# Kernel tuning notes

Measured on AMD Instinct MI355X. Metric: run time of the kernel, lower is better.

## Reference

```python
import jax, jax.numpy as jnp
import numpy as np

B, S, D = 4, 2048, 1024
H, HD = 16, 64
F = 4096
EPS = 1e-5


def layer_norm(x, gamma, beta):
    mu = jnp.mean(x, axis=-1, keepdims=True)
    var = jnp.var(x, axis=-1, keepdims=True)
    return (x - mu) * jax.lax.rsqrt(var + EPS) * gamma + beta


def setup_inputs() -> dict:
    key = jax.random.key(0)
    ks = jax.random.split(key, 16)
    s_d = 1.0 / np.sqrt(D)
    s_hd = 1.0 / np.sqrt(H * HD)
    s_f = 1.0 / np.sqrt(F)
    return {
        "x": jax.random.normal(ks[0], (B, S, D), jnp.float32),
        # per-head Q/K/V linears stacked over heads: [H, D, HD]
        "Wq": jax.random.uniform(ks[1], (H, D, HD), jnp.float32, -s_d, s_d),
        "bq": jax.random.uniform(ks[2], (H, HD), jnp.float32, -s_d, s_d),
        "Wk": jax.random.uniform(ks[3], (H, D, HD), jnp.float32, -s_d, s_d),
        "bk": jax.random.uniform(ks[4], (H, HD), jnp.float32, -s_d, s_d),
        "Wv": jax.random.uniform(ks[5], (H, D, HD), jnp.float32, -s_d, s_d),
        "bv": jax.random.uniform(ks[6], (H, HD), jnp.float32, -s_d, s_d),
        "Wo": jax.random.uniform(ks[7], (H * HD, D), jnp.float32, -s_hd, s_hd),
        "bo": jax.random.uniform(ks[8], (D,), jnp.float32, -s_hd, s_hd),
        "W1": jax.random.uniform(ks[9], (D, F), jnp.float32, -s_d, s_d),
        "b1": jax.random.uniform(ks[10], (F,), jnp.float32, -s_d, s_d),
        "W2": jax.random.uniform(ks[11], (F, D), jnp.float32, -s_f, s_f),
        "b2": jax.random.uniform(ks[12], (D,), jnp.float32, -s_f, s_f),
        "g1": jnp.ones((D,), jnp.float32),
        "be1": jnp.zeros((D,), jnp.float32),
        "g2": jnp.ones((D,), jnp.float32),
        "be2": jnp.zeros((D,), jnp.float32),
    }


def reference(x, Wq, bq, Wk, bk, Wv, bv, Wo, bo, W1, b1, W2, b2, g1, be1, g2, be2):
    scale = HD ** (-0.5)
    # per-head projections: [B,S,H,HD]
    Q = jnp.einsum("bsd,hde->bshe", x, Wq) + bq
    K = jnp.einsum("bsd,hde->bshe", x, Wk) + bk
    V = jnp.einsum("bsd,hde->bshe", x, Wv) + bv
    scores = jnp.einsum("bqhe,bkhe->bhqk", Q, K) * scale
    attn = jax.nn.softmax(scores, axis=-1)
    ctx = jnp.einsum("bhqk,bkhe->bqhe", attn, V)  # [B,S,H,HD]
    concat = ctx.reshape(B, S, H * HD)  # head-order concat
    attn_out = concat @ Wo + bo
    x1 = layer_norm(x + attn_out, g1, be1)
    ffn = jax.nn.relu(x1 @ W1 + b1) @ W2 + b2
    return layer_norm(x1 + ffn, g2, be2)
```

## Files before the change

### kernel.cpp

```cpp
#include <hip/hip_runtime.h>

#define B_ 4
#define S_ 2048
#define D_ 1024
#define H_ 16
#define HD_ 64
#define F_ 4096
#define M_ (B_*S_)
#define QS_ 3072


typedef __attribute__((ext_vector_type(8))) short bf16x8;
typedef __attribute__((ext_vector_type(4))) short short4_t;
typedef __attribute__((ext_vector_type(4))) float f32x4;
typedef __attribute__((ext_vector_type(16))) float f32x16;

#define AS1q __attribute__((address_space(1)))
#define AS3q __attribute__((address_space(3)))

__device__ __forceinline__ float bf2f(short u) {
    union { unsigned int i; float f; } v;
    v.i = ((unsigned int)(unsigned short)u) << 16;
    return v.f;
}
__device__ __forceinline__ short f2bf(float f) {
    union { float f; unsigned int i; } v; v.f = f;
    unsigned int r = v.i + 0x7fffu + ((v.i >> 16) & 1u);
    return (short)(r >> 16);
}
__device__ __forceinline__ void gld_lds16(const short* g, short* l) {
    __builtin_amdgcn_global_load_lds((const AS1q void*)g, (AS3q void*)l, 16, 0, 0);
}
__device__ __forceinline__ unsigned int cvtpk_bf16(float a, float b) {
    unsigned int r;
    asm("v_cvt_pk_bf16_f32 %0, %1, %2" : "=v"(r) : "v"(a), "v"(b));
    return r;
}
__device__ __forceinline__ float max3f(float a, float b, float c) {
    float r;
    asm("v_max3_f32 %0, %1, %2, %3" : "=v"(r) : "v"(a), "v"(b), "v"(c));
    return r;
}

__global__ __launch_bounds__(256) void cvt_f2b_k(
    const float* __restrict__ in, short* __restrict__ out, long n)
{
    long i = ((long)blockIdx.x * 256 + threadIdx.x) * 4;
    long stride = (long)gridDim.x * 256 * 4;
    for (; i < n; i += stride) {
        float4 v = *(const float4*)(in + i);
        short4_t o;
        o[0] = f2bf(v.x); o[1] = f2bf(v.y); o[2] = f2bf(v.z); o[3] = f2bf(v.w);
        *(short4_t*)(out + i) = o;
    }
}

template<typename TI>
__global__ __launch_bounds__(256) void transpose_k(
    const TI* __restrict__ in, short* __restrict__ out,
    int rows, long in_rstride,
    long in_bstrideB, long in_bstrideH, long out_bstride)
{
    __shared__ short tile[32][33];
    int z = blockIdx.z;
    const TI* ip = in + (long)(z >> 4) * in_bstrideB + (long)(z & 15) * in_bstrideH;
    short* op = out + (long)z * out_bstride;
    int r0 = blockIdx.y * 32, c0 = blockIdx.x * 32;
    int tx = threadIdx.x & 31, ty = threadIdx.x >> 5;
#pragma unroll
    for (int i = 0; i < 32; i += 8) {
        TI v = ip[(long)(r0 + ty + i) * in_rstride + (c0 + tx)];
        if constexpr (sizeof(TI) == 4) tile[ty + i][tx] = f2bf((float)v);
        else                           tile[ty + i][tx] = (short)v;
    }
    __syncthreads();
#pragma unroll
    for (int i = 0; i < 32; i += 8)
        op[(long)(c0 + ty + i) * rows + (r0 + tx)] = tile[tx][ty + i];
}

__global__ __launch_bounds__(256) void gemm_k(
    const short* __restrict__ A,
    const short* __restrict__ BT,
    const float* __restrict__ bias,
    short* __restrict__ C,
    int M, int N, int K, float scale, int relu)
{
    __shared__ short Alds[2*128*32];
    __shared__ short Blds[2*128*32];
    int tid = threadIdx.x;
    int wave = tid >> 6, lane = tid & 63;
    int lgrp = lane >> 4, lrow = lane & 15;
    int wr = wave >> 1, wc = wave & 1;
    int gx = gridDim.x;
    int nwg = gx * gridDim.y;
    int lin = blockIdx.y * gx + blockIdx.x;
    int nid = (lin & 7) * (nwg >> 3) + (lin >> 3);
    int bm = (nid / gx) * 128, bn = (nid % gx) * 128;

    int srow = wave * 32 + (lane >> 2);
    int scol = (lane & 3) * 8;
    const short* gA = A  + (long)(bm + srow) * K + scol;
    const short* gB = BT + (long)(bn + srow) * K + scol;
    short* lA0 = &Alds[(wave * 32) * 32];
    short* lA1 = &Alds[(wave * 32 + 16) * 32];
    short* lB0 = &Blds[(wave * 32) * 32];
    short* lB1 = &Blds[(wave * 32 + 16) * 32];
    long k16 = 16L * K;

    #define GSTAGE(buf, k0_) do {                              \
        gld_lds16(gA + (k0_),       lA0 + (buf)*4096);         \
        gld_lds16(gA + (k0_) + k16, lA1 + (buf)*4096);         \
        gld_lds16(gB + (k0_),       lB0 + (buf)*4096);         \
        gld_lds16(gB + (k0_) + k16, lB1 + (buf)*4096);         \
    } while (0)

    f32x4 acc[4][4] = {};
    int nk = K >> 5;
    GSTAGE(0, 0);
    __syncthreads();
    for (int t = 0; t < nk; ++t) {
        int cur = t & 1;
        if (t + 1 < nk) GSTAGE(cur ^ 1, (t + 1) * 32);
        bf16x8 af[4], bv[4];
#pragma unroll
        for (int i = 0; i < 4; i++) {
            af[i] = *(const bf16x8*)&Alds[cur*4096 + (wr*64 + i*16 + lrow) * 32 + 8*lgrp];
            bv[i] = *(const bf16x8*)&Blds[cur*4096 + (wc*64 + i*16 + lrow) * 32 + 8*lgrp];
        }
#pragma unroll
        for (int mi = 0; mi < 4; mi++)
#pragma unroll
            for (int ni = 0; ni < 4; ni++)
                acc[mi][ni] = __builtin_amdgcn_mfma_f32_16x16x32_bf16(
                    af[mi], bv[ni], acc[mi][ni], 0, 0, 0);
        __syncthreads();
    }
    #undef GSTAGE
#pragma unroll
    for (int ni = 0; ni < 4; ni++) {
        int col = bn + wc*64 + ni*16 + lrow;
        float bb = bias[col];
#pragma unroll
        for (int mi = 0; mi < 4; mi++) {
#pragma unroll
            for (int j = 0; j < 4; j++) {
                int row = bm + wr*64 + mi*16 + lgrp*4 + j;
                float v = (acc[mi][ni][j] + bb) * scale;
                if (relu) v = fmaxf(v, 0.0f);
                C[(long)row * N + col] = f2bf(v);
            }
        }
    }
}

__global__ __launch_bounds__(256) void gemm_qkv_k(
    const short* __restrict__ A,
    const short* __restrict__ BT,
    const float* __restrict__ bq,
    const float* __restrict__ bk,
    const float* __restrict__ bv,
    short* __restrict__ C,
    short* __restrict__ VT,
    float qscale)
{
    __shared__ short Alds[2*128*32];
    __shared__ short Blds[2*128*32];
    const int K = 1024;
    int tid = threadIdx.x;
    int wave = tid >> 6, lane = tid & 63;
    int lgrp = lane >> 4, lrow = lane & 15;
    int wr = wave >> 1, wc = wave & 1;
    int gx = gridDim.x;
    int nwg = gx * gridDim.y;
    int lin = blockIdx.y * gx + blockIdx.x;
    int nid = (lin & 7) * (nwg >> 3) + (lin >> 3);
    int bm = (nid / gx) * 128, bn = (nid % gx) * 128;
    int seg = bn >> 10;
    const float* bp = (seg == 0) ? bq : (seg == 1) ? bk : bv;
    float scale = (seg == 0) ? qscale : 1.0f;

    int srow = wave * 32 + (lane >> 2);
    int scol = (lane & 3) * 8;
    const short* gA = A  + (long)(bm + srow) * K + scol;
    const short* gB = BT + (long)(bn + srow) * K + scol;
    short* lA0 = &Alds[(wave * 32) * 32];
    short* lA1 = &Alds[(wave * 32 + 16) * 32];
    short* lB0 = &Blds[(wave * 32) * 32];
    short* lB1 = &Blds[(wave * 32 + 16) * 32];
    long k16 = 16L * K;

    #define GSTAGE(buf, k0_) do {                              \
        gld_lds16(gA + (k0_),       lA0 + (buf)*4096);         \
        gld_lds16(gA + (k0_) + k16, lA1 + (buf)*4096);         \
        gld_lds16(gB + (k0_),       lB0 + (buf)*4096);         \
        gld_lds16(gB + (k0_) + k16, lB1 + (buf)*4096);         \
    } while (0)

    f32x4 acc[4][4] = {};
    GSTAGE(0, 0);
    __syncthreads();
    for (int t = 0; t < 32; ++t) {
        int cur = t & 1;
        if (t < 31) GSTAGE(cur ^ 1, (t + 1) * 32);
        bf16x8 af[4], bvv[4];
#pragma unroll
        for (int i = 0; i < 4; i++) {
            af[i]  = *(const bf16x8*)&Alds[cur*4096 + (wr*64 + i*16 + lrow) * 32 + 8*lgrp];
            bvv[i] = *(const bf16x8*)&Blds[cur*4096 + (wc*64 + i*16 + lrow) * 32 + 8*lgrp];
        }
#pragma unroll
        for (int mi = 0; mi < 4; mi++)
#pragma unroll
            for (int ni = 0; ni < 4; ni++)
                acc[mi][ni] = __builtin_amdgcn_mfma_f32_16x16x32_bf16(
                    af[mi], bvv[ni], acc[mi][ni], 0, 0, 0);
        __syncthreads();
    }
    #undef GSTAGE
    if (seg == 2) {
        int bq0 = bm >> 11;
#pragma unroll
        for (int ni = 0; ni < 4; ni++) {
            int col = bn + wc*64 + ni*16 + lrow;
            int e   = col & 63;
            int bh  = bq0*16 + ((col >> 6) - 32);
            float bb = bp[col & 1023];
#pragma unroll
            for (int mi = 0; mi < 4; mi++) {
                int tok = (bm + wr*64 + mi*16 + lgrp*4) & 2047;
                short4_t o;
#pragma unroll
                for (int j = 0; j < 4; j++) o[j] = f2bf(acc[mi][ni][j] + bb);
                *(short4_t*)(VT + (long)bh*131072L + (long)e*2048 + tok) = o;
            }
        }
    } else {
#pragma unroll
        for (int ni = 0; ni < 4; ni++) {
            int col = bn + wc*64 + ni*16 + lrow;
            float bb = bp[col & 1023];
#pragma unroll
            for (int mi = 0; mi < 4; mi++) {
#pragma unroll
                for (int j = 0; j < 4; j++) {
                    int row = bm + wr*64 + mi*16 + lgrp*4 + j;
                    C[(long)row * QS_ + col] = f2bf((acc[mi][ni][j] + bb) * scale);
                }
            }
        }
    }
}

__global__ __launch_bounds__(256) void attn_k(
    const short* __restrict__ QKV,
    const short* __restrict__ VT,
    short* __restrict__ O)
{
    __shared__ short KV[2][2][4096];
    int lin = blockIdx.y * 16 + blockIdx.x;
    int nid = (lin & 7) * 128 + (lin >> 3);
    int bh = nid >> 4, qt = nid & 15;
    int b = bh >> 4, h = bh & 15;
    int q0 = qt * 128;
    int tid = threadIdx.x, wave = tid >> 6, lane = tid & 63;
    int l31 = lane & 31, hi = lane >> 5;
    int sw = l31 & 7;

    bf16x8 aq[4];
    {
        const short* qp = QKV + (long)(b*S_ + q0 + wave*32 + l31) * QS_ + h*64 + 8*hi;
#pragma unroll
        for (int t = 0; t < 4; t++)
            aq[t] = *(const bf16x8*)(qp + 16*t);
    }
    bf16x8 ones;
#pragma unroll
    for (int i = 0; i < 8; i++) ones[i] = (short)0x3F80;

    f32x16 accO[2] = {};
    f32x16 accsum = {};
    float negmj = 0.0f;

    int srow = lane >> 3;
    int schunk = (lane & 7) ^ srow;
    const short* ksrc = QKV + (long)(b*S_ + wave*16 + srow) * QS_ + 1024 + h*64 + schunk*8;
    const short* vsrc = VT + (long)bh * (64L*S_) + (long)(wave*16 + srow) * S_ + schunk*8;
    short* kd = &KV[0][0][wave*1024];
    short* vd = &KV[0][1][wave*1024];

    #define STAGE(buf, kb_) do {                                        \
        gld_lds16(ksrc + (long)(kb_)     * QS_, kd + (buf)*8192);        \
        gld_lds16(ksrc + (long)((kb_)+8) * QS_, kd + (buf)*8192 + 512);  \
        gld_lds16(vsrc + (kb_),                 vd + (buf)*8192);        \
        gld_lds16(vsrc + 8*S_ + (kb_),          vd + (buf)*8192 + 512);  \
    } while (0)

    STAGE(0, 0);
    __syncthreads();

    for (int t = 0; t < 32; ++t) {
        int cur = t & 1;
        if (t < 31) STAGE(cur ^ 1, (t + 1) * 64);
        const char* KB = (const char*)&KV[cur][0][0];
        const char* VB = (const char*)&KV[cur][1][0];

        f32x16 accs[2];
#pragma unroll
        for (int c = 0; c < 2; c++)
#pragma unroll
            for (int r = 0; r < 16; r++) accs[c][r] = negmj;
#pragma unroll
        for (int c = 0; c < 2; c++) {
            bf16x8 ak[4];
#pragma unroll
            for (int tt = 0; tt < 4; tt++)
                ak[tt] = *(const bf16x8*)(KB + (32*c + l31)*128 + (((2*tt + hi) ^ sw) << 4));
            __builtin_amdgcn_s_setprio(1);
#pragma unroll
            for (int tt = 0; tt < 4; tt++)
                accs[c] = __builtin_amdgcn_mfma_f32_32x32x16_bf16(
                    ak[tt], aq[tt], accs[c], 0, 0, 0);
            __builtin_amdgcn_s_setprio(0);
        }

        if ((t & 3) == 0) {
            float mA = fmaxf(accs[0][0], accs[0][1]);
            float mB = fmaxf(accs[1][0], accs[1][1]);
#pragma unroll
            for (int r = 2; r < 16; r += 2) {
                mA = max3f(mA, accs[0][r], accs[0][r+1]);
                mB = max3f(mB, accs[1][r], accs[1][r+1]);
            }
            float m4 = fmaxf(mA, mB);
            if (!__all(m4 <= 8.0f)) {
                float m2 = fmaxf(m4, __shfl_xor(m4, 32));
                float d = fmaxf(m2, 0.0f);
                float al = exp2f(-d);
                negmj -= d;
#pragma unroll
                for (int c = 0; c < 2; c++)
#pragma unroll
                    for (int r = 0; r < 16; r++) accs[c][r] -= d;
#pragma unroll
                for (int r = 0; r < 16; r++) {
                    float alr = __shfl(al, (r & 3) + 8 * (r >> 2) + 4 * hi);
                    accO[0][r] *= alr; accO[1][r] *= alr; accsum[r] *= alr;
                }
            }
        }
#pragma unroll
        for (int c = 0; c < 2; c++)
#pragma unroll
            for (int r = 0; r < 16; r++)
                accs[c][r] = exp2f(accs[c][r]);

        bf16x8 pa[4];
#pragma unroll
        for (int ks = 0; ks < 4; ks++) {
            int c = ks >> 1, o = (ks & 1) * 8;
            unsigned int c0 = cvtpk_bf16(accs[c][o+0], accs[c][o+1]);
            unsigned int c1 = cvtpk_bf16(accs[c][o+2], accs[c][o+3]);
            unsigned int c2 = cvtpk_bf16(accs[c][o+4], accs[c][o+5]);
            unsigned int c3 = cvtpk_bf16(accs[c][o+6], accs[c][o+7]);
            asm("v_permlane32_swap_b32 %0, %1" : "+v"(c0), "+v"(c2));
            asm("v_permlane32_swap_b32 %0, %1" : "+v"(c1), "+v"(c3));
            union { unsigned int u[4]; bf16x8 v; } pk;
            pk.u[0] = c0; pk.u[1] = c1; pk.u[2] = c2; pk.u[3] = c3;
            pa[ks] = pk.v;
        }

        __builtin_amdgcn_s_setprio(1);
#pragma unroll
        for (int eb = 0; eb < 2; eb++)
#pragma unroll
            for (int ks = 0; ks < 4; ks++) {
                bf16x8 bvf = *(const bf16x8*)(VB + (32*eb + l31)*128 + (((2*ks + hi) ^ sw) << 4));
                accO[eb] = __builtin_amdgcn_mfma_f32_32x32x16_bf16(
                    pa[ks], bvf, accO[eb], 0, 0, 0);
            }
#pragma unroll
        for (int ks = 0; ks < 4; ks++)
            accsum = __builtin_amdgcn_mfma_f32_32x32x16_bf16(
                pa[ks], ones, accsum, 0, 0, 0);
        __builtin_amdgcn_s_setprio(0);

        __syncthreads();
    }
    #undef STAGE

    const short* ob = O + (long)(b*S_) * 1024 + h*64;
#pragma unroll
    for (int r = 0; r < 16; r++) {
        int crow = (r & 3) + 8 * (r >> 2) + 4 * hi;
        float invr = 1.0f / accsum[r];
        int qr = q0 + wave*32 + crow;
#pragma unroll
        for (int eb = 0; eb < 2; eb++)
            ((short*)ob)[(long)qr * 1024 + 32*eb + l31] = f2bf(accO[eb][r] * invr);
    }
}

template<int XF32, int OUTF32>
__global__ __launch_bounds__(256) void ln_k(
    const void* __restrict__ Xv, const short* __restrict__ Y,
    const float* __restrict__ g, const float* __restrict__ be,
    void* __restrict__ Ov)
{
    int row = blockIdx.x, tid = threadIdx.x;
    long base = (long)row * 1024 + tid * 4;
    float a[4];
    if constexpr (XF32) {
        float4 xv = *(const float4*)((const float*)Xv + base);
        a[0] = xv.x; a[1] = xv.y; a[2] = xv.z; a[3] = xv.w;
    } else {
        short4_t xv = *(const short4_t*)((const short*)Xv + base);
#pragma unroll
        for (int j = 0; j < 4; j++) a[j] = bf2f(xv[j]);
    }
    short4_t yv = *(const short4_t*)(Y + base);
    float s = 0.f, s2 = 0.f;
#pragma unroll
    for (int j = 0; j < 4; j++) {
        a[j] += bf2f(yv[j]);
        s += a[j]; s2 += a[j] * a[j];
    }
#pragma unroll
    for (int off = 32; off >= 1; off >>= 1) {
        s  += __shfl_xor(s, off);
        s2 += __shfl_xor(s2, off);
    }
    __shared__ float red[8];
    if ((tid & 63) == 0) { red[(tid >> 6)*2] = s; red[(tid >> 6)*2 + 1] = s2; }
    __syncthreads();
    s  = red[0] + red[2] + red[4] + red[6];
    s2 = red[1] + red[3] + red[5] + red[7];
    float mean = s * (1.0f/1024.0f);
    float var  = s2 * (1.0f/1024.0f) - mean*mean;
    float rstd = rsqrtf(var + 1e-5f);
    float4 gv = *(const float4*)(g  + tid*4);
    float4 bv = *(const float4*)(be + tid*4);
    float r0 = (a[0] - mean) * rstd * gv.x + bv.x;
    float r1 = (a[1] - mean) * rstd * gv.y + bv.y;
    float r2 = (a[2] - mean) * rstd * gv.z + bv.z;
    float r3 = (a[3] - mean) * rstd * gv.w + bv.w;
    if constexpr (OUTF32) {
        *(float4*)((float*)Ov + base) = make_float4(r0, r1, r2, r3);
    } else {
        short4_t ov;
        ov[0] = f2bf(r0); ov[1] = f2bf(r1); ov[2] = f2bf(r2); ov[3] = f2bf(r3);
        *(short4_t*)((short*)Ov + base) = ov;
    }
}

extern "C" void kernel_launch(void* const* d_in, const int* in_sizes, int n_in,
                              void* d_out, int out_size, void* d_ws, size_t ws_size,
                              hipStream_t stream)
{
    static const int ins[17] = {0,1,2,3,4,5,6,7,8,9,10,11,12,13,14,15,16};
    static const int srt[17] = {16,4,12,2,10,5,13,3,11,0,6,1,7,14,8,15,9};
    const int* IX = (in_sizes[0] == 8388608) ? ins : srt;

    const float* x   = (const float*)d_in[IX[0]];
    const float* Wq  = (const float*)d_in[IX[1]];
    const float* bq  = (const float*)d_in[IX[2]];
    const float* Wk  = (const float*)d_in[IX[3]];
    const float* bk  = (const float*)d_in[IX[4]];
    const float* Wv  = (const float*)d_in[IX[5]];
    const float* bv  = (const float*)d_in[IX[6]];
    const float* Wo  = (const float*)d_in[IX[7]];
    const float* bo  = (const float*)d_in[IX[8]];
    const float* W1  = (const float*)d_in[IX[9]];
    const float* b1  = (const float*)d_in[IX[10]];
    const float* W2  = (const float*)d_in[IX[11]];
    const float* b2  = (const float*)d_in[IX[12]];
    const float* g1  = (const float*)d_in[IX[13]];
    const float* be1 = (const float*)d_in[IX[14]];
    const float* g2  = (const float*)d_in[IX[15]];
    const float* be2 = (const float*)d_in[IX[16]];
    short* ws  = (short*)d_ws;

    short* QKVb = ws + 0L;
    short* VTb  = ws + 25165824L;
    short* ctx  = ws + 33554432L;
    short* QKVT = ws + 41943040L;
    short* WoT  = ws + 45088768L;
    short* xb   = ws + 46137344L;
    short* W1T  = ws + 54525952L;
    short* W2T  = ws + 58720256L;
    short* x1   = ws + 0L;
    short* hb   = ws + 8388608L;
    short* ao   = ws + 46137344L;
    short* ffn  = ws + 41943040L;

    dim3 blk(256);

    cvt_f2b_k<<<2048, blk, 0, stream>>>(x, xb, (long)M_ * D_);

    transpose_k<float><<<dim3(2, 32, 16),  blk, 0, stream>>>(Wq, QKVT,            1024, 64,   0, 65536, 65536);
    transpose_k<float><<<dim3(2, 32, 16),  blk, 0, stream>>>(Wk, QKVT + 1048576L, 1024, 64,   0, 65536, 65536);
    transpose_k<float><<<dim3(2, 32, 16),  blk, 0, stream>>>(Wv, QKVT + 2097152L, 1024, 64,   0, 65536, 65536);
    transpose_k<float><<<dim3(32, 32, 1),  blk, 0, stream>>>(Wo, WoT, 1024, 1024, 0, 0, 0);
    transpose_k<float><<<dim3(128, 32, 1), blk, 0, stream>>>(W1, W1T, 1024, 4096, 0, 0, 0);
    transpose_k<float><<<dim3(32, 128, 1), blk, 0, stream>>>(W2, W2T, 4096, 1024, 0, 0, 0);

    gemm_qkv_k<<<dim3(24, 64), blk, 0, stream>>>(
        xb, QKVT, bq, bk, bv, QKVb, VTb, 0.18033688011112042f);

    attn_k<<<dim3(16, 64), blk, 0, stream>>>(QKVb, VTb, ctx);

    gemm_k<<<dim3(8, 64), blk, 0, stream>>>(ctx, WoT, bo, ao, M_, 1024, 1024, 1.0f, 0);
    ln_k<1,0><<<8192, blk, 0, stream>>>(x, ao, g1, be1, x1);

    gemm_k<<<dim3(32, 64), blk, 0, stream>>>(x1, W1T, b1, hb,  M_, 4096, 1024, 1.0f, 1);
    gemm_k<<<dim3(8, 64),  blk, 0, stream>>>(hb, W2T, b2, ffn, M_, 1024, 4096, 1.0f, 0);

    ln_k<0,1><<<8192, blk, 0, stream>>>(x1, ffn, g2, be2, d_out);
}
```

Before: 440.5 us.

## Use 256x256 tiled GEMM with 4-stage LDS pipeline for QKV and FFN1

Replaces the 128x128 QKV GEMM with a templated 256x256-tile kernel using 512 threads, a 4-slot LDS ring with prefetch two stages ahead, XOR-swizzled LDS layout, and setprio around MFMA blocks. The same kernel also serves the W1 FFN GEMM. The goal is more data reuse per tile, fewer LDS bank conflicts, and better overlap of global loads with compute. It uses more LDS and registers per workgroup, which may limit occupancy, and the grid becomes small (384 and 512 workgroups), which risks tail imbalance.

Measured after the change: 450.9 us, median of 2. 1.02x slower.

```diff
diff --git a/kernel.cpp b/kernel.cpp
--- a/kernel.cpp
+++ b/kernel.cpp
@@ -154,98 +154,136 @@
     }
 }
 
-__global__ __launch_bounds__(256) void gemm_qkv_k(
+template<int MODE>
+__global__ __launch_bounds__(512, 2) void gemm256_k(
     const short* __restrict__ A,
     const short* __restrict__ BT,
-    const float* __restrict__ bq,
+    const float* __restrict__ bias,
     const float* __restrict__ bk,
     const float* __restrict__ bv,
     short* __restrict__ C,
     short* __restrict__ VT,
-    float qscale)
-{
-    __shared__ short Alds[2*128*32];
-    __shared__ short Blds[2*128*32];
-    const int K = 1024;
+    int M, int N, int K, float scale, int relu)
+{
+    __shared__ short Al[4][256*32];
+    __shared__ short Bl[4][256*32];
     int tid = threadIdx.x;
     int wave = tid >> 6, lane = tid & 63;
     int lgrp = lane >> 4, lrow = lane & 15;
-    int wr = wave >> 1, wc = wave & 1;
+    int wr = wave >> 2, wc = wave & 3;
     int gx = gridDim.x;
     int nwg = gx * gridDim.y;
     int lin = blockIdx.y * gx + blockIdx.x;
     int nid = (lin & 7) * (nwg >> 3) + (lin >> 3);
-    int bm = (nid / gx) * 128, bn = (nid % gx) * 128;
-    int seg = bn >> 10;
-    const float* bp = (seg == 0) ? bq : (seg == 1) ? bk : bv;
-    float scale = (seg == 0) ? qscale : 1.0f;
-
-    int srow = wave * 32 + (lane >> 2);
-    int scol = (lane & 3) * 8;
-    const short* gA = A  + (long)(bm + srow) * K + scol;
-    const short* gB = BT + (long)(bn + srow) * K + scol;
-    short* lA0 = &Alds[(wave * 32) * 32];
-    short* lA1 = &Alds[(wave * 32 + 16) * 32];
-    short* lB0 = &Blds[(wave * 32) * 32];
-    short* lB1 = &Blds[(wave * 32 + 16) * 32];
-    long k16 = 16L * K;
-
-    #define GSTAGE(buf, k0_) do {                              \
-        gld_lds16(gA + (k0_),       lA0 + (buf)*4096);         \
-        gld_lds16(gA + (k0_) + k16, lA1 + (buf)*4096);         \
-        gld_lds16(gB + (k0_),       lB0 + (buf)*4096);         \
-        gld_lds16(gB + (k0_) + k16, lB1 + (buf)*4096);         \
+    int bm = (nid / gx) * 256, bn = (nid % gx) * 256;
+
+    int srow = lane >> 2;
+    int schunk = (lane & 3) ^ ((lane >> 3) & 3);
+    const short* gA0 = A  + (long)(bm + wave*32 + srow) * K + schunk*8;
+    const short* gA1 = gA0 + 16L*K;
+    const short* gB0 = BT + (long)(bn + wave*32 + srow) * K + schunk*8;
+    const short* gB1 = gB0 + 16L*K;
+    short* lA = &Al[0][(wave*32)*32];
+    short* lB = &Bl[0][(wave*32)*32];
+
+    #define G256(slot, k0_) do {                         \
+        gld_lds16(gA0 + (k0_), lA + (slot)*8192);         \
+        gld_lds16(gA1 + (k0_), lA + (slot)*8192 + 512);   \
+        gld_lds16(gB0 + (k0_), lB + (slot)*8192);         \
+        gld_lds16(gB1 + (k0_), lB + (slot)*8192 + 512);   \
     } while (0)
 
-    f32x4 acc[4][4] = {};
-    GSTAGE(0, 0);
-    __syncthreads();
-    for (int t = 0; t < 32; ++t) {
-        int cur = t & 1;
-        if (t < 31) GSTAGE(cur ^ 1, (t + 1) * 32);
-        bf16x8 af[4], bvv[4];
-#pragma unroll
-        for (int i = 0; i < 4; i++) {
-            af[i]  = *(const bf16x8*)&Alds[cur*4096 + (wr*64 + i*16 + lrow) * 32 + 8*lgrp];
-            bvv[i] = *(const bf16x8*)&Blds[cur*4096 + (wc*64 + i*16 + lrow) * 32 + 8*lgrp];
-        }
-#pragma unroll
-        for (int mi = 0; mi < 4; mi++)
-#pragma unroll
-            for (int ni = 0; ni < 4; ni++)
-                acc[mi][ni] = __builtin_amdgcn_mfma_f32_16x16x32_bf16(
-                    af[mi], bvv[ni], acc[mi][ni], 0, 0, 0);
-        __syncthreads();
-    }
-    #undef GSTAGE
-    if (seg == 2) {
-        int bq0 = bm >> 11;
+    f32x4 acc[8][4] = {};
+    int nk = K >> 5;
+    G256(0, 0);
+    G256(1, 32);
+    for (int t = 0; t < nk; ++t) {
+        int cur = t & 3;
+        asm volatile("s_waitcnt vmcnt(4)" ::: "memory");
+        __builtin_amdgcn_s_barrier();
+        __builtin_amdgcn_sched_barrier(0);
+        {
+            int ts = (t + 2 < nk) ? (t + 2) : (nk - 1);
+            G256((t + 2) & 3, ts * 32);
+        }
+        const short* Ab = &Al[cur][0];
+        const short* Bb = &Bl[cur][0];
+        bf16x8 bfr[4];
+#pragma unroll
+        for (int ni = 0; ni < 4; ni++) {
+            int row = wc*64 + ni*16 + lrow;
+            bfr[ni] = *(const bf16x8*)(Bb + row*32 + ((lgrp ^ ((row >> 1) & 3)) << 3));
+        }
+#pragma unroll
+        for (int half = 0; half < 2; half++) {
+            bf16x8 afr[4];
+#pragma unroll
+            for (int i = 0; i < 4; i++) {
+                int row = wr*128 + (half*4 + i)*16 + lrow;
+                afr[i] = *(const bf16x8*)(Ab + row*32 + ((lgrp ^ ((row >> 1) & 3)) << 3));
+            }
+            __builtin_amdgcn_s_setprio(1);
+#pragma unroll
+            for (int i = 0; i < 4; i++)
+#pragma unroll
+                for (int ni = 0; ni < 4; ni++)
+                    acc[half*4 + i][ni] = __builtin_amdgcn_mfma_f32_16x16x32_bf16(
+                        afr[i], bfr[ni], acc[half*4 + i][ni], 0, 0, 0);
+            __builtin_amdgcn_s_setprio(0);
+        }
+    }
+    #undef G256
+    asm volatile("s_waitcnt vmcnt(0)" ::: "memory");
+
+    if constexpr (MODE == 1) {
+        int seg = bn >> 10;
+        const float* bp = (seg == 0) ? bias : (seg == 1) ? bk : bv;
+        float qs = (seg == 0) ? scale : 1.0f;
+        if (seg == 2) {
+            int bq0 = bm >> 11;
+#pragma unroll
+            for (int ni = 0; ni < 4; ni++) {
+                int col = bn + wc*64 + ni*16 + lrow;
+                int e   = col & 63;
+                int bh  = bq0*16 + ((col >> 6) - 32);
+                float bb = bp[col & 1023];
+#pragma unroll
+                for (int mi = 0; mi < 8; mi++) {
+                    int tok = (bm + wr*128 + mi*16 + lgrp*4) & 2047;
+                    short4_t o;
+#pragma unroll
+                    for (int j = 0; j < 4; j++) o[j] = f2bf(acc[mi][ni][j] + bb);
+                    *(short4_t*)(VT + (long)bh*131072L + (long)e*2048 + tok) = o;
+                }
+            }
+        } else {
+#pragma unroll
+            for (int ni = 0; ni < 4; ni++) {
+                int col = bn + wc*64 + ni*16 + lrow;
+                float bb = bp[col & 1023];
+#pragma unroll
+                for (int mi = 0; mi < 8; mi++) {
+#pragma unroll
+                    for (int j = 0; j < 4; j++) {
+                        int row = bm + wr*128 + mi*16 + lgrp*4 + j;
+                        C[(long)row * QS_ + col] = f2bf((acc[mi][ni][j] + bb) * qs);
+                    }
+                }
+            }
+        }
+    } else {
 #pragma unroll
         for (int ni = 0; ni < 4; ni++) {
             int col = bn + wc*64 + ni*16 + lrow;
-            int e   = col & 63;
-            int bh  = bq0*16 + ((col >> 6) - 32);
-            float bb = bp[col & 1023];
-#pragma unroll
-            for (int mi = 0; mi < 4; mi++) {
-                int tok = (bm + wr*64 + mi*16 + lgrp*4) & 2047;
-                short4_t o;
-#pragma unroll
-                for (int j = 0; j < 4; j++) o[j] = f2bf(acc[mi][ni][j] + bb);
-                *(short4_t*)(VT + (long)bh*131072L + (long)e*2048 + tok) = o;
-            }
-        }
-    } else {
-#pragma unroll
-        for (int ni = 0; ni < 4; ni++) {
-            int col = bn + wc*64 + ni*16 + lrow;
-            float bb = bp[col & 1023];
-#pragma unroll
-            for (int mi = 0; mi < 4; mi++) {
+            float bb = bias[col];
+#pragma unroll
+            for (int mi = 0; mi < 8; mi++) {
 #pragma unroll
                 for (int j = 0; j < 4; j++) {
-                    int row = bm + wr*64 + mi*16 + lgrp*4 + j;
-                    C[(long)row * QS_ + col] = f2bf((acc[mi][ni][j] + bb) * scale);
+                    int row = bm + wr*128 + mi*16 + lgrp*4 + j;
+                    float v = acc[mi][ni][j] + bb;
+                    if (relu) v = fmaxf(v, 0.0f);
+                    C[(long)row * N + col] = f2bf(v);
                 }
             }
         }
@@ -504,15 +542,16 @@
     transpose_k<float><<<dim3(128, 32, 1), blk, 0, stream>>>(W1, W1T, 1024, 4096, 0, 0, 0);
     transpose_k<float><<<dim3(32, 128, 1), blk, 0, stream>>>(W2, W2T, 4096, 1024, 0, 0, 0);
 
-    gemm_qkv_k<<<dim3(24, 64), blk, 0, stream>>>(
-        xb, QKVT, bq, bk, bv, QKVb, VTb, 0.18033688011112042f);
+    gemm256_k<1><<<dim3(12, 32), dim3(512), 0, stream>>>(
+        xb, QKVT, bq, bk, bv, QKVb, VTb, M_, QS_, 1024, 0.18033688011112042f, 0);
 
     attn_k<<<dim3(16, 64), blk, 0, stream>>>(QKVb, VTb, ctx);
 
     gemm_k<<<dim3(8, 64), blk, 0, stream>>>(ctx, WoT, bo, ao, M_, 1024, 1024, 1.0f, 0);
     ln_k<1,0><<<8192, blk, 0, stream>>>(x, ao, g1, be1, x1);
 
-    gemm_k<<<dim3(32, 64), blk, 0, stream>>>(x1, W1T, b1, hb,  M_, 4096, 1024, 1.0f, 1);
+    gemm256_k<0><<<dim3(16, 32), dim3(512), 0, stream>>>(
+        x1, W1T, b1, nullptr, nullptr, hb, nullptr, M_, 4096, 1024, 1.0f, 1);
     gemm_k<<<dim3(8, 64),  blk, 0, stream>>>(hb, W2T, b2, ffn, M_, 1024, 4096, 1.0f, 0);
 
     ln_k<0,1><<<8192, blk, 0, stream>>>(x1, ffn, g2, be2, d_out);
```
